# Performance work log

Hardware: AMD Instinct MI355X
Metric: run time of the kernel (lower is better)

## Reference

```python
import jax, jax.numpy as jnp
import numpy as np

B, T, D, H, DH, M, L, OUT = 512, 49, 256, 8, 32, 1024, 4, 151
DI = H * DH
THR = 0.02


def _ln(x, g, b):
    mu = x.mean(-1, keepdims=True)
    v = ((x - mu) ** 2).mean(-1, keepdims=True)
    return (x - mu) / jnp.sqrt(v + 1e-5) * g + b


def setup_inputs() -> dict:
    key = jax.random.key(0)
    ks = iter(jax.random.split(key, 64))

    def W(*s):
        return jax.random.normal(next(ks), s, jnp.float32) * 0.02

    inp = {}
    for n in ['img0', 'img1', 'p0', 'p1', 'p2']:
        inp[n] = jax.random.normal(next(ks), (B, T, D), jnp.float32)
    inp['idx'] = jax.random.randint(next(ks), (3, 2, B, T), 0, T, dtype=jnp.int32)
    # two transformer encoders (image/point), stacked over [encoder=2, layer=L]
    inp['enc_ln1g'] = jnp.ones((2, L, D)); inp['enc_ln1b'] = jnp.zeros((2, L, D))
    inp['enc_wqkv'] = W(2, L, D, 3 * DI)
    inp['enc_wo'] = W(2, L, DI, D); inp['enc_bo'] = jnp.zeros((2, L, D))
    inp['enc_ln2g'] = jnp.ones((2, L, D)); inp['enc_ln2b'] = jnp.zeros((2, L, D))
    inp['enc_w1'] = W(2, L, D, M); inp['enc_b1'] = jnp.zeros((2, L, M))
    inp['enc_w2'] = W(2, L, M, D); inp['enc_b2'] = jnp.zeros((2, L, D))
    # per-depth score nets (PredictorLG)
    inp['sc_lng'] = jnp.ones((L, D)); inp['sc_lnb'] = jnp.zeros((L, D))
    inp['sc_w1'] = W(L, D, D); inp['sc_b1'] = jnp.zeros((L, D))
    inp['sc_w2'] = W(L, D, D // 2); inp['sc_b2'] = jnp.zeros((L, D // 2))
    inp['sc_w3'] = W(L, D // 2, 2); inp['sc_b3'] = jnp.zeros((L, 2))
    # per-depth patch MLPs (FFN dim->mlp_dim->mlp_dim->dim, 3 layers)
    inp['pm_w1'] = W(L, D, M); inp['pm_b1'] = jnp.zeros((L, M))
    inp['pm_w2'] = W(L, M, M); inp['pm_b2'] = jnp.zeros((L, M))
    inp['pm_w3'] = W(L, M, D); inp['pm_b3'] = jnp.zeros((L, D))
    # mlp head
    inp['hd_lng'] = jnp.ones((D,)); inp['hd_lnb'] = jnp.zeros((D,))
    inp['hd_w1'] = W(D, M); inp['hd_b1'] = jnp.zeros((M,))
    inp['hd_w2'] = W(M, OUT); inp['hd_b2'] = jnp.zeros((OUT,))
    return inp


def reference(img0, img1, p0, p1, p2, idx,
              enc_ln1g, enc_ln1b, enc_wqkv, enc_wo, enc_bo,
              enc_ln2g, enc_ln2b, enc_w1, enc_b1, enc_w2, enc_b2,
              sc_lng, sc_lnb, sc_w1, sc_b1, sc_w2, sc_b2, sc_w3, sc_b3,
              pm_w1, pm_b1, pm_w2, pm_b2, pm_w3, pm_b3,
              hd_lng, hd_lnb, hd_w1, hd_b1, hd_w2, hd_b2):

    def layer(x, e, i):
        # pre-norm attention
        h = _ln(x, enc_ln1g[e, i], enc_ln1b[e, i])
        qkv = h @ enc_wqkv[e, i]                      # [B,T,3*DI]
        q, k, v = jnp.split(qkv, 3, axis=-1)
        q = q.reshape(B, T, H, DH); k = k.reshape(B, T, H, DH); v = v.reshape(B, T, H, DH)
        a = jax.nn.softmax(jnp.einsum('bqhd,bkhd->bhqk', q, k) * (DH ** -0.5), -1)
        o = jnp.einsum('bhqk,bkhd->bqhd', a, v).reshape(B, T, DI)
        x = x + o @ enc_wo[e, i] + enc_bo[e, i]
        # pre-norm FFN
        h = _ln(x, enc_ln2g[e, i], enc_ln2b[e, i])
        return x + jax.nn.gelu(h @ enc_w1[e, i] + enc_b1[e, i]) @ enc_w2[e, i] + enc_b2[e, i]

    image_feats = [img0, img1]
    point_feats = [p0, p1, p2]
    pred_scores = []
    for i in range(L):
        image_tokens = [layer(f, 0, i) for f in image_feats]
        point_tokens = [layer(f, 1, i) for f in point_feats]
        allt = jnp.concatenate(image_tokens + point_tokens, axis=1)  # [B, 5*T, D]
        h = _ln(allt, sc_lng[i], sc_lnb[i])
        h = jax.nn.gelu(h @ sc_w1[i] + sc_b1[i])
        h = jax.nn.gelu(h @ sc_w2[i] + sc_b2[i])
        scores = jax.nn.softmax(h @ sc_w3[i] + sc_b3[i], -1)[:, :, 0]  # [B, 5*T]
        pred_scores.append(scores)
        mask = (scores > THR).astype(jnp.int32)[..., None]            # [B,5*T,1]
        fm = mask.astype(allt.dtype)
        fnm = (-mask - 1).astype(allt.dtype)  # torch ~int_mask is bitwise NOT: ~1=-2, ~0=-1 (faithful)
        image_feats = [image_tokens[j] * fm[:, j * T:(j + 1) * T]
                       + image_tokens[1 - j] * fnm[:, j * T:(j + 1) * T] for j in range(2)]

        def patch_mlp(x):
            h2 = jax.nn.gelu(x @ pm_w1[i] + pm_b1[i])
            h2 = jax.nn.gelu(h2 @ pm_w2[i] + pm_b2[i])
            return h2 @ pm_w3[i] + pm_b3[i]

        new_p = []
        for k2 in range(3):
            s0 = 2 * T + k2 * T
            g0 = jnp.take_along_axis(image_tokens[0], idx[k2, 0][..., None], axis=1)
            g1 = jnp.take_along_axis(image_tokens[1], idx[k2, 1][..., None], axis=1)
            patch = patch_mlp(g0) + patch_mlp(g1)
            new_p.append(point_tokens[k2] * fm[:, s0:s0 + T] + patch * fnm[:, s0:s0 + T])
        point_feats = new_p

    pooled = jnp.concatenate(image_feats + point_feats, axis=1).max(axis=1)  # [B, D]
    h = _ln(pooled, hd_lng, hd_lnb)
    smplx = jax.nn.gelu(h @ hd_w1 + hd_b1) @ hd_w2 + hd_b2                   # [B, OUT]
    pred_score = jnp.concatenate(pred_scores, axis=1)                         # [B, L*5*T]
    return smplx, pred_score
```

## Files before the change

### kernel.cpp

```cpp
#include <hip/hip_runtime.h>
#include <math.h>

#define B_ 512
#define T_ 49
#define D_ 256
#define M_ 1024
#define L_ 4
#define OUT_ 151
#define BT_ 25088
#define NTOK5 (5*BT_)
#define THRESH 0.02f

typedef __bf16 bf16x8 __attribute__((ext_vector_type(8)));
typedef float f32x4 __attribute__((ext_vector_type(4)));
typedef unsigned short us;

__device__ __forceinline__ float gelu_t(float x){
    float u = 0.7978845608028654f * x * (1.0f + 0.044715f*x*x);
    float e = __expf(-2.0f*u);
    return __fdividef(x, 1.0f + e);
}
__device__ __forceinline__ us f2bf(float f){
    unsigned int u = __float_as_uint(f);
    u += 0x7fffu + ((u>>16)&1u);
    return (us)(u>>16);
}
__device__ __forceinline__ float bf2f(us h){
    return __uint_as_float(((unsigned int)h)<<16);
}
__device__ __forceinline__ void gload16(const void* g, void* l){
    __builtin_amdgcn_global_load_lds(
        (const __attribute__((address_space(1))) void*)g,
        (__attribute__((address_space(3))) void*)l, 16, 0, 0);
}

__global__ void copy_in_kernel(const float* __restrict__ a0, const float* __restrict__ a1,
                               const float* __restrict__ a2, const float* __restrict__ a3,
                               const float* __restrict__ a4, float* __restrict__ dst){
    size_t i = (size_t)blockIdx.x*256 + threadIdx.x;
    if (i >= (size_t)NTOK5*64) return;
    int slot = (int)(i / ((size_t)BT_*64));
    size_t off = i % ((size_t)BT_*64);
    const float* src = slot==0?a0: slot==1?a1: slot==2?a2: slot==3?a3: a4;
    ((float4*)dst)[i] = ((const float4*)src)[off];
}

__global__ void xcvt_kernel(const float* __restrict__ x, us* __restrict__ y, int nrows){
    size_t i = (size_t)blockIdx.x*256 + threadIdx.x;
    if (i >= (size_t)nrows*64) return;
    float4 v = ((const float4*)x)[i];
    ushort4 o; o.x=f2bf(v.x); o.y=f2bf(v.y); o.z=f2bf(v.z); o.w=f2bf(v.w);
    ((ushort4*)y)[i] = o;
}

template<bool OBF>
__global__ void ln_kernel(const float* __restrict__ x, const float* __restrict__ g,
                          const float* __restrict__ b, void* __restrict__ y, int nrows){
    int row = blockIdx.x*4 + (threadIdx.x>>6);
    if (row >= nrows) return;
    int lane = threadIdx.x & 63;
    float4 v = ((const float4*)(x + (size_t)row*D_))[lane];
    float s  = v.x+v.y+v.z+v.w;
    float sq = v.x*v.x + v.y*v.y + v.z*v.z + v.w*v.w;
    #pragma unroll
    for (int o=32;o;o>>=1){ s += __shfl_xor(s,o,64); sq += __shfl_xor(sq,o,64); }
    float mu = s*(1.0f/256.0f);
    float rstd = rsqrtf(sq*(1.0f/256.0f) - mu*mu + 1e-5f);
    float4 gv = ((const float4*)g)[lane];
    float4 bv = ((const float4*)b)[lane];
    float o0 = (v.x-mu)*rstd*gv.x + bv.x;
    float o1 = (v.y-mu)*rstd*gv.y + bv.y;
    float o2 = (v.z-mu)*rstd*gv.z + bv.z;
    float o3 = (v.w-mu)*rstd*gv.w + bv.w;
    if (OBF){
        ushort4 o4; o4.x=f2bf(o0); o4.y=f2bf(o1); o4.z=f2bf(o2); o4.w=f2bf(o3);
        ((ushort4*)((us*)y + (size_t)row*D_))[lane] = o4;
    } else {
        float4 o4; o4.x=o0; o4.y=o1; o4.z=o2; o4.w=o3;
        ((float4*)((float*)y + (size_t)row*D_))[lane] = o4;
    }
}

__global__ void wtrans_kernel(const float* __restrict__ W, us* __restrict__ Wt,
                              int K, int N){
    int g = blockIdx.z;
    __shared__ float t[32][33];
    int k0 = blockIdx.y*32, n0 = blockIdx.x*32;
    int tx = threadIdx.x&31, ty = threadIdx.x>>5;
    for (int r=ty; r<32; r+=8){
        int k = k0+r, n = n0+tx;
        t[r][tx] = (k<K && n<N) ? W[(size_t)g*K*N + (size_t)k*N + n] : 0.f;
    }
    __syncthreads();
    for (int r=ty; r<32; r+=8){
        int n = n0+r, k = k0+tx;
        if (n<N && k<K) Wt[(size_t)g*N*K + (size_t)n*K + k] = f2bf(t[tx][r]);
    }
}

__global__ void wtrans_pad_kernel(const float* __restrict__ W, us* __restrict__ Wt,
                                  int K, int Nsrc, int Ndst){
    __shared__ float t[32][33];
    int k0 = blockIdx.y*32, n0 = blockIdx.x*32;
    int tx = threadIdx.x&31, ty = threadIdx.x>>5;
    for (int r=ty; r<32; r+=8){
        int k = k0+r, n = n0+tx;
        t[r][tx] = (k<K && n<Nsrc) ? W[(size_t)k*Nsrc + n] : 0.f;
    }
    __syncthreads();
    for (int r=ty; r<32; r+=8){
        int n = n0+r, k = k0+tx;
        if (n<Ndst && k<K) Wt[(size_t)n*K + k] = f2bf(t[tx][r]);
    }
}

__global__ void padb_kernel(const float* __restrict__ b, float* __restrict__ o,
                            int Nsrc, int Ndst){
    int i = blockIdx.x*256 + threadIdx.x;
    if (i < Ndst) o[i] = (i < Nsrc) ? b[i] : 0.f;
}

__global__ void headcopy_kernel(const float* __restrict__ src, float* __restrict__ dst){
    int i = blockIdx.x*256 + threadIdx.x;
    if (i >= B_*OUT_) return;
    int r = i / OUT_, c = i % OUT_;
    dst[i] = src[(size_t)r*256 + c];
}

__device__ __forceinline__ void gemm_compute(const us* As, const us* Bs,
        int wr, int wc, int lr, int kg, f32x4 (&acc)[4][4]){
    bf16x8 av[4], bv[4];
    #pragma unroll
    for (int mi=0;mi<4;mi++){
        int r = wr*64 + mi*16 + lr;
        av[mi] = *(const bf16x8*)(&As[r*32 + ((kg ^ ((r>>1)&3))<<3)]);
    }
    #pragma unroll
    for (int ni=0;ni<4;ni++){
        int c = wc*64 + ni*16 + lr;
        bv[ni] = *(const bf16x8*)(&Bs[c*32 + ((kg ^ ((c>>1)&3))<<3)]);
    }
    #pragma unroll
    for (int mi=0;mi<4;mi++)
        #pragma unroll
        for (int ni=0;ni<4;ni++)
            acc[mi][ni] = __builtin_amdgcn_mfma_f32_16x16x32_bf16(av[mi], bv[ni], acc[mi][ni], 0, 0, 0);
}

template<int ACT, int RIN, bool OBF>
__global__ __launch_bounds__(256) void mfma_gemm(
    const us* __restrict__ A, const us* __restrict__ Wt,
    const float* __restrict__ bias, const void* __restrict__ resid,
    void* __restrict__ Cout, int Mr, int N, int K)
{
    __shared__ __align__(16) us SM[2*8192];
    const int nwg  = gridDim.x*gridDim.y;
    const int flat = blockIdx.y*gridDim.x + blockIdx.x;
    const int qq = nwg>>3, rr = nwg&7;
    const int xcd = flat&7, sidx = flat>>3;
    const int logical = (xcd<rr) ? (xcd*(qq+1)+sidx) : (rr*(qq+1)+(xcd-rr)*qq+sidx);
    const int bn = (logical % gridDim.x)*128;
    const int bm = (logical / gridDim.x)*128;
    const int tid = threadIdx.x;
    const int lane = tid&63, w = tid>>6;
    const int wr = w>>1, wc = w&1;
    const int lr = lane&15, kg = lane>>4;
    f32x4 acc[4][4] = {};

    const int j0 = tid, j1 = tid+256;
    const int row0 = j0>>2, row1 = j1>>2;
    const int k8s0 = (j0&3) ^ ((row0>>1)&3);
    const int k8s1 = (j1&3) ^ ((row1>>1)&3);
    int ga0 = bm+row0; if (ga0>=Mr) ga0=Mr-1;
    int ga1 = bm+row1; if (ga1>=Mr) ga1=Mr-1;
    int gb0 = bn+row0; if (gb0>=N) gb0=N-1;
    int gb1 = bn+row1; if (gb1>=N) gb1=N-1;
    const us* a0p = A  + (size_t)ga0*K + k8s0*8;
    const us* a1p = A  + (size_t)ga1*K + k8s1*8;
    const us* b0p = Wt + (size_t)gb0*K + k8s0*8;
    const us* b1p = Wt + (size_t)gb1*K + k8s1*8;

    const int nk = K >> 5;
    {
        us* b0 = SM;
        gload16(a0p, b0 + j0*8);
        gload16(a1p, b0 + j1*8);
        gload16(b0p, b0 + 4096 + j0*8);
        gload16(b1p, b0 + 4096 + j1*8);
        us* b1 = SM + 8192;
        gload16(a0p+32, b1 + j0*8);
        gload16(a1p+32, b1 + j1*8);
        gload16(b0p+32, b1 + 4096 + j0*8);
        gload16(b1p+32, b1 + 4096 + j1*8);
    }
    int cur = 0;
    for (int t=0; t<nk-1; ++t){
        asm volatile("s_waitcnt vmcnt(4)" ::: "memory");
        __builtin_amdgcn_s_barrier();
        __builtin_amdgcn_sched_barrier(0);
        const us* cbase = SM + cur*8192;
        gemm_compute(cbase, cbase+4096, wr, wc, lr, kg, acc);
        __builtin_amdgcn_sched_barrier(0);
        __builtin_amdgcn_s_barrier();
        if (t+2 < nk){
            us* nbase = SM + cur*8192;
            int k0 = (t+2)<<5;
            gload16(a0p+k0, nbase + j0*8);
            gload16(a1p+k0, nbase + j1*8);
            gload16(b0p+k0, nbase + 4096 + j0*8);
            gload16(b1p+k0, nbase + 4096 + j1*8);
        }
        cur ^= 1;
    }
    asm volatile("s_waitcnt vmcnt(0)" ::: "memory");
    __builtin_amdgcn_s_barrier();
    __builtin_amdgcn_sched_barrier(0);
    {
        const us* cbase = SM + cur*8192;
        gemm_compute(cbase, cbase+4096, wr, wc, lr, kg, acc);
    }
    __syncthreads();

    if (OBF && RIN==0){
        us* Cs16 = (us*)SM;
        #pragma unroll
        for (int mi=0;mi<4;mi++){
            #pragma unroll
            for (int ni=0;ni<4;ni++){
                #pragma unroll
                for (int r4=0;r4<4;r4++){
                    int row = wr*64 + mi*16 + kg*4 + r4;
                    int col = wc*64 + ni*16 + lr;
                    float v = acc[mi][ni][r4];
                    if (bias) v += bias[bn + col];
                    if (ACT==1) v = gelu_t(v);
                    int h = ((row>>2)&3) | ((row&1)<<2);
                    int punit = (col>>3) ^ h;
                    Cs16[row*128 + punit*8 + (col&7)] = f2bf(v);
                }
            }
        }
        __syncthreads();
        {
            int rbase = tid>>3, seg = tid&7;
            #pragma unroll
            for (int pass=0; pass<8; ++pass){
                int row = rbase + (pass>>1)*32;
                int half = pass&1;
                int grow = bm + row;
                if (grow < Mr){
                    int h = ((row>>2)&3) | ((row&1)<<2);
                    int punit = (half*8+seg) ^ h;
                    *(uint4*)((us*)Cout + (size_t)grow*N + bn + half*64 + seg*8)
                        = *(const uint4*)&Cs16[row*128 + punit*8];
                }
            }
        }
        return;
    }

    float* Cs = (float*)SM;
    #pragma unroll
    for (int er=0; er<2; er++){
        #pragma unroll
        for (int ml=0; ml<2; ml++){
            int mi = er*2 + ml;
            #pragma unroll
            for (int ni=0;ni<4;ni++){
                #pragma unroll
                for (int r4=0;r4<4;r4++){
                    int lrow = wr*32 + ml*16 + kg*4 + r4;
                    int lcol = wc*64 + ni*16 + lr;
                    int pcol = lcol ^ (((lrow>>2)&1)<<4);
                    float v = acc[mi][ni][r4];
                    if (bias) v += bias[bn + lcol];
                    if (ACT==1) v = gelu_t(v);
                    Cs[lrow*128 + pcol] = v;
                }
            }
        }
        __syncthreads();
        #pragma unroll
        for (int s=0; s<2; s++){
            int lrow = (tid>>3) + s*32;
            int tseg = tid&7;
            int pseg = tseg ^ ((lrow>>2)&1);
            const float4* src = (const float4*)&Cs[lrow*128 + pseg*16];
            float4 v0=src[0], v1=src[1], v2=src[2], v3=src[3];
            int grow = bm + (lrow>>5)*64 + (er*2 + ((lrow>>4)&1))*16 + (lrow&15);
            int gcol = bn + tseg*16;
            if (grow < Mr){
                if (RIN==1){
                    const float4* rp = (const float4*)((const float*)resid + (size_t)grow*N + gcol);
                    float4 r0=rp[0], r1=rp[1], r2=rp[2], r3=rp[3];
                    v0.x+=r0.x; v0.y+=r0.y; v0.z+=r0.z; v0.w+=r0.w;
                    v1.x+=r1.x; v1.y+=r1.y; v1.z+=r1.z; v1.w+=r1.w;
                    v2.x+=r2.x; v2.y+=r2.y; v2.z+=r2.z; v2.w+=r2.w;
                    v3.x+=r3.x; v3.y+=r3.y; v3.z+=r3.z; v3.w+=r3.w;
                } else if (RIN==2){
                    const uint4* rp = (const uint4*)((const us*)resid + (size_t)grow*N + gcol);
                    uint4 u0=rp[0], u1=rp[1];
                    v0.x+=bf2f((us)(u0.x&0xffff)); v0.y+=bf2f((us)(u0.x>>16));
                    v0.z+=bf2f((us)(u0.y&0xffff)); v0.w+=bf2f((us)(u0.y>>16));
                    v1.x+=bf2f((us)(u0.z&0xffff)); v1.y+=bf2f((us)(u0.z>>16));
                    v1.z+=bf2f((us)(u0.w&0xffff)); v1.w+=bf2f((us)(u0.w>>16));
                    v2.x+=bf2f((us)(u1.x&0xffff)); v2.y+=bf2f((us)(u1.x>>16));
                    v2.z+=bf2f((us)(u1.y&0xffff)); v2.w+=bf2f((us)(u1.y>>16));
                    v3.x+=bf2f((us)(u1.z&0xffff)); v3.y+=bf2f((us)(u1.z>>16));
                    v3.z+=bf2f((us)(u1.w&0xffff)); v3.w+=bf2f((us)(u1.w>>16));
                }
                if (OBF){
                    unsigned int w0 = (unsigned)f2bf(v0.x) | ((unsigned)f2bf(v0.y)<<16);
                    unsigned int w1 = (unsigned)f2bf(v0.z) | ((unsigned)f2bf(v0.w)<<16);
                    unsigned int w2 = (unsigned)f2bf(v1.x) | ((unsigned)f2bf(v1.y)<<16);
                    unsigned int w3 = (unsigned)f2bf(v1.z) | ((unsigned)f2bf(v1.w)<<16);
                    unsigned int w4 = (unsigned)f2bf(v2.x) | ((unsigned)f2bf(v2.y)<<16);
                    unsigned int w5 = (unsigned)f2bf(v2.z) | ((unsigned)f2bf(v2.w)<<16);
                    unsigned int w6 = (unsigned)f2bf(v3.x) | ((unsigned)f2bf(v3.y)<<16);
                    unsigned int w7 = (unsigned)f2bf(v3.z) | ((unsigned)f2bf(v3.w)<<16);
                    uint4* op = (uint4*)((us*)Cout + (size_t)grow*N + gcol);
                    uint4 u0; u0.x=w0; u0.y=w1; u0.z=w2; u0.w=w3;
                    uint4 u1; u1.x=w4; u1.y=w5; u1.z=w6; u1.w=w7;
                    op[0]=u0; op[1]=u1;
                } else {
                    float4* op = (float4*)((float*)Cout + (size_t)grow*N + gcol);
                    op[0]=v0; op[1]=v1; op[2]=v2; op[3]=v3;
                }
            }
        }
        __syncthreads();
    }
}

__global__ void attn_kernel(const us* __restrict__ qkv, us* __restrict__ o){
    int bb = blockIdx.x >> 3;
    int h  = blockIdx.x & 7;
    __shared__ float qs[49][33], ks[49][33], vs[49][33];
    __shared__ float ss[49][49];
    const us* base = qkv + (size_t)bb*T_*768 + h*32;
    for (int i = threadIdx.x; i < 49*16; i += 256){
        int t = i>>4, d2 = i&15;
        unsigned int q = *(const unsigned int*)(base + (size_t)t*768 + d2*2);
        unsigned int k = *(const unsigned int*)(base + (size_t)t*768 + 256 + d2*2);
        unsigned int v = *(const unsigned int*)(base + (size_t)t*768 + 512 + d2*2);
        qs[t][d2*2] = bf2f((us)(q&0xffff)); qs[t][d2*2+1] = bf2f((us)(q>>16));
        ks[t][d2*2] = bf2f((us)(k&0xffff)); ks[t][d2*2+1] = bf2f((us)(k>>16));
        vs[t][d2*2] = bf2f((us)(v&0xffff)); vs[t][d2*2+1] = bf2f((us)(v>>16));
    }
    __syncthreads();
    for (int i = threadIdx.x; i < 49*49; i += 256){
        int r = i/49, c = i%49;
        float acc = 0.f;
        #pragma unroll
        for (int d=0;d<32;d++) acc += qs[r][d]*ks[c][d];
        ss[r][c] = acc*0.17677669529663687f;
    }
    __syncthreads();
    if (threadIdx.x < 196){
        int r = threadIdx.x>>2, q = threadIdx.x&3;
        float m = -1e30f;
        for (int c=q; c<49; c+=4) m = fmaxf(m, ss[r][c]);
        m = fmaxf(m, __shfl_xor(m,1,64)); m = fmaxf(m, __shfl_xor(m,2,64));
        float sum = 0.f;
        for (int c=q; c<49; c+=4){ float e = __expf(ss[r][c]-m); ss[r][c]=e; sum+=e; }
        sum += __shfl_xor(sum,1,64); sum += __shfl_xor(sum,2,64);
        float inv = __fdividef(1.0f, sum);
        for (int c=q; c<49; c+=4) ss[r][c] *= inv;
    }
    __syncthreads();
    for (int i = threadIdx.x; i < 49*32; i += 256){
        int r = i>>5, d = i&31;
        float acc = 0.f;
        for (int c=0;c<49;c++) acc += ss[r][c]*vs[c][d];
        o[((size_t)bb*T_ + r)*256 + h*32 + d] = f2bf(acc);
    }
}

__global__ void score_kernel(const us* __restrict__ s2, const float* __restrict__ w3,
                             const float* __restrict__ b3, float* __restrict__ sc,
                             float* __restrict__ pred, int layer, int row0, int nrows){
    int lr = blockIdx.x*256 + threadIdx.x;
    if (lr >= nrows) return;
    int row = row0 + lr;
    int s = row / BT_;
    int r = row % BT_;
    int b = r / T_;
    int t = r % T_;
    const uint4* xv = (const uint4*)(s2 + (size_t)lr*128);
    float l0 = b3[0], l1 = b3[1];
    #pragma unroll
    for (int q=0;q<16;q++){
        uint4 u = xv[q];
        unsigned int uu[4] = {u.x,u.y,u.z,u.w};
        #pragma unroll
        for (int e=0;e<4;e++){
            float fa = bf2f((us)(uu[e]&0xffff));
            float fb = bf2f((us)(uu[e]>>16));
            int d = q*8 + e*2;
            l0 += fa*w3[d*2]     + fb*w3[(d+1)*2];
            l1 += fa*w3[d*2+1]   + fb*w3[(d+1)*2+1];
        }
    }
    float m = fmaxf(l0,l1);
    float e0 = __expf(l0-m), e1 = __expf(l1-m);
    float sc0 = __fdividef(e0, e0+e1);
    sc[b*(5*T_) + s*T_ + t] = sc0;
    pred[(size_t)b*(L_*5*T_) + (size_t)layer*(5*T_) + s*T_ + t] = sc0;
}

__global__ void img_fuse_kernel(float* __restrict__ X, const float* __restrict__ sc){
    size_t i = (size_t)blockIdx.x*256 + threadIdx.x;
    if (i >= (size_t)BT_*64) return;
    int row = (int)(i>>6), d4 = (int)(i&63);
    int b = row / T_, t = row % T_;
    float s0 = sc[b*(5*T_) + t];
    float s1 = sc[b*(5*T_) + T_ + t];
    float fm0  = (s0 > THRESH)? 1.f : 0.f;
    float fnm0 = -fm0 - 1.f;
    float fm1  = (s1 > THRESH)? 1.f : 0.f;
    float fnm1 = -fm1 - 1.f;
    float4* p0 = ((float4*)(X + (size_t)row*D_)) + d4;
    float4* p1 = ((float4*)(X + ((size_t)BT_ + row)*D_)) + d4;
    float4 a0 = *p0, a1 = *p1;
    float4 r0, r1;
    r0.x = a0.x*fm0 + a1.x*fnm0;  r0.y = a0.y*fm0 + a1.y*fnm0;
    r0.z = a0.z*fm0 + a1.z*fnm0;  r0.w = a0.w*fm0 + a1.w*fnm0;
    r1.x = a1.x*fm1 + a0.x*fnm1;  r1.y = a1.y*fm1 + a0.y*fnm1;
    r1.z = a1.z*fm1 + a0.z*fnm1;  r1.w = a1.w*fm1 + a0.w*fnm1;
    *p0 = r0; *p1 = r1;
}

__global__ void pt_fuse_gather_kernel(float* __restrict__ X, const us* __restrict__ PM,
                                      const int* __restrict__ idx, const float* __restrict__ sc){
    size_t i = (size_t)blockIdx.x*256 + threadIdx.x;
    if (i >= (size_t)3*BT_*64) return;
    int vrow = (int)(i>>6), d4 = (int)(i&63);
    int k2 = vrow / BT_, grow = vrow % BT_;
    int b = grow / T_, t = grow % T_;
    float s = sc[b*(5*T_) + (2+k2)*T_ + t];
    float fm  = (s > THRESH)? 1.f : 0.f;
    float fnm = -fm - 1.f;
    int i0 = idx[(size_t)(k2*2+0)*BT_ + grow];
    int i1 = idx[(size_t)(k2*2+1)*BT_ + grow];
    uint2 u0 = ((const uint2*)(PM + ((size_t)b*T_ + i0)*D_))[d4];
    uint2 u1 = ((const uint2*)(PM + ((size_t)BT_ + (size_t)b*T_ + i1)*D_))[d4];
    float p0 = bf2f((us)(u0.x&0xffff)) + bf2f((us)(u1.x&0xffff));
    float p1 = bf2f((us)(u0.x>>16))    + bf2f((us)(u1.x>>16));
    float p2 = bf2f((us)(u0.y&0xffff)) + bf2f((us)(u1.y&0xffff));
    float p3 = bf2f((us)(u0.y>>16))    + bf2f((us)(u1.y>>16));
    float4* xp = ((float4*)(X + ((size_t)(2+k2)*BT_ + grow)*D_)) + d4;
    float4 a = *xp;
    float4 rr;
    rr.x = a.x*fm + p0*fnm;
    rr.y = a.y*fm + p1*fnm;
    rr.z = a.z*fm + p2*fnm;
    rr.w = a.w*fm + p3*fnm;
    *xp = rr;
}

__global__ void pool_kernel(const float* __restrict__ x, float* __restrict__ p){
    int i = blockIdx.x*256 + threadIdx.x;
    if (i >= B_*64) return;
    int b = i>>6, d4 = i&63;
    float4 m; m.x=m.y=m.z=m.w=-3.4e38f;
    for (int s=0;s<5;s++){
        const float4* bp = ((const float4*)(x + ((size_t)s*BT_ + (size_t)b*T_)*D_)) + d4;
        for (int t=0;t<T_;t++){
            float4 v = bp[(size_t)t*64];
            m.x=fmaxf(m.x,v.x); m.y=fmaxf(m.y,v.y); m.z=fmaxf(m.z,v.z); m.w=fmaxf(m.w,v.w);
        }
    }
    ((float4*)p)[i] = m;
}

static inline int cdiv(int a, int b){ return (a+b-1)/b; }

extern "C" void kernel_launch(void* const* d_in, const int* in_sizes, int n_in,
                              void* d_out, int out_size, void* d_ws, size_t ws_size,
                              hipStream_t stream)
{
    const float* in_img0 = (const float*)d_in[0];
    const float* in_img1 = (const float*)d_in[1];
    const float* in_p0   = (const float*)d_in[2];
    const float* in_p1   = (const float*)d_in[3];
    const float* in_p2   = (const float*)d_in[4];
    const int*   in_idx  = (const int*)d_in[5];
    const float* enc_ln1g = (const float*)d_in[6];
    const float* enc_ln1b = (const float*)d_in[7];
    const float* enc_wqkv = (const float*)d_in[8];
    const float* enc_wo   = (const float*)d_in[9];
    const float* enc_bo   = (const float*)d_in[10];
    const float* enc_ln2g = (const float*)d_in[11];
    const float* enc_ln2b = (const float*)d_in[12];
    const float* enc_w1   = (const float*)d_in[13];
    const float* enc_b1   = (const float*)d_in[14];
    const float* enc_w2   = (const float*)d_in[15];
    const float* enc_b2   = (const float*)d_in[16];
    const float* sc_lng   = (const float*)d_in[17];
    const float* sc_lnb   = (const float*)d_in[18];
    const float* sc_w1    = (const float*)d_in[19];
    const float* sc_b1    = (const float*)d_in[20];
    const float* sc_w2    = (const float*)d_in[21];
    const float* sc_b2    = (const float*)d_in[22];
    const float* sc_w3    = (const float*)d_in[23];
    const float* sc_b3    = (const float*)d_in[24];
    const float* pm_w1    = (const float*)d_in[25];
    const float* pm_b1    = (const float*)d_in[26];
    const float* pm_w2    = (const float*)d_in[27];
    const float* pm_b2    = (const float*)d_in[28];
    const float* pm_w3    = (const float*)d_in[29];
    const float* pm_b3    = (const float*)d_in[30];
    const float* hd_lng   = (const float*)d_in[31];
    const float* hd_lnb   = (const float*)d_in[32];
    const float* hd_w1    = (const float*)d_in[33];
    const float* hd_b1    = (const float*)d_in[34];
    const float* hd_w2    = (const float*)d_in[35];
    const float* hd_b2    = (const float*)d_in[36];

    char* p = (char*)d_ws;
    float* X   = (float*)p;  p += (size_t)5*BT_*D_*4;
    float* SCb = (float*)p;  p += (size_t)B_*5*T_*4;
    us* PM   = (us*)p; p += (size_t)2*BT_*D_*2;
    us* WQKV = (us*)p; p += (size_t)8*768*256*2;
    us* WWO  = (us*)p; p += (size_t)8*256*256*2;
    us* WW1  = (us*)p; p += (size_t)8*1024*256*2;
    us* WW2  = (us*)p; p += (size_t)8*256*1024*2;
    us* WS1  = (us*)p; p += (size_t)4*256*256*2;
    us* WS2  = (us*)p; p += (size_t)4*128*256*2;
    us* WP1  = (us*)p; p += (size_t)4*1024*256*2;
    us* WP2  = (us*)p; p += (size_t)4*1024*1024*2;
    us* WP3  = (us*)p; p += (size_t)4*256*1024*2;
    us* WH1  = (us*)p; p += (size_t)1024*256*2;
    us* WH2  = (us*)p; p += (size_t)256*1024*2;
    float* B2P  = (float*)p; p += (size_t)256*4;
    float* POOL = (float*)p; p += (size_t)B_*256*4;
    us*    HLNb = (us*)p;  p += (size_t)B_*256*2;
    us*    HMIDb= (us*)p;  p += (size_t)B_*1024*2;
    float* HOUT = (float*)p; p += (size_t)B_*256*4;
    size_t fixed = (size_t)(p - (char*)d_ws);
    long long pool = (long long)ws_size - (long long)fixed;
    if (pool < 0) pool = 0;
    auto chunkOf = [&](long long perRow, int maxRows)->int{
        long long c = pool / perRow;
        c = (c / T_) * T_;
        if (c < T_) c = T_;
        if (c > maxRows) c = maxRows;
        return (int)c;
    };
    int Cenc = chunkOf(3072, 3*BT_);
    int Csc  = chunkOf(1280, NTOK5);
    int Cpm  = chunkOf(4608, 2*BT_);
    char* pb = p;
    us* eR1 = (us*)pb;
    us* eR2 = (us*)(pb + (size_t)Cenc*512);
    us* eR3 = (us*)(pb + (size_t)Cenc*512 + (size_t)Cenc*2048);
    us* sR1 = (us*)pb;
    us* sS1 = (us*)(pb + (size_t)Csc*512);
    us* sS2 = (us*)(pb + (size_t)Csc*1024);
    us* cA  = (us*)pb;
    us* m1  = (us*)(pb + (size_t)Cpm*512);
    us* m2  = (us*)(pb + (size_t)Cpm*512 + (size_t)Cpm*2048);

    float* out_smplx = (float*)d_out;
    float* out_pred  = out_smplx + (size_t)B_*OUT_;

    wtrans_kernel<<<dim3(cdiv(768,32), cdiv(256,32), 8),256,0,stream>>>(enc_wqkv, WQKV, 256, 768);
    wtrans_kernel<<<dim3(cdiv(256,32), cdiv(256,32), 8),256,0,stream>>>(enc_wo,   WWO,  256, 256);
    wtrans_kernel<<<dim3(cdiv(1024,32),cdiv(256,32), 8),256,0,stream>>>(enc_w1,   WW1,  256, 1024);
    wtrans_kernel<<<dim3(cdiv(256,32), cdiv(1024,32),8),256,0,stream>>>(enc_w2,   WW2,  1024,256);
    wtrans_kernel<<<dim3(cdiv(256,32), cdiv(256,32), 4),256,0,stream>>>(sc_w1,    WS1,  256, 256);
    wtrans_kernel<<<dim3(cdiv(128,32), cdiv(256,32), 4),256,0,stream>>>(sc_w2,    WS2,  256, 128);
    wtrans_kernel<<<dim3(cdiv(1024,32),cdiv(256,32), 4),256,0,stream>>>(pm_w1,    WP1,  256, 1024);
    wtrans_kernel<<<dim3(cdiv(1024,32),cdiv(1024,32),4),256,0,stream>>>(pm_w2,    WP2,  1024,1024);
    wtrans_kernel<<<dim3(cdiv(256,32), cdiv(1024,32),4),256,0,stream>>>(pm_w3,    WP3,  1024,256);
    wtrans_kernel<<<dim3(cdiv(1024,32),cdiv(256,32), 1),256,0,stream>>>(hd_w1,    WH1,  256, 1024);
    wtrans_pad_kernel<<<dim3(cdiv(256,32), cdiv(1024,32)),256,0,stream>>>(hd_w2, WH2, 1024, 151, 256);
    padb_kernel<<<1,256,0,stream>>>(hd_b2, B2P, 151, 256);

    copy_in_kernel<<<cdiv(NTOK5*64,256), 256, 0, stream>>>(in_img0,in_img1,in_p0,in_p1,in_p2, X);

    for (int i=0;i<L_;i++){
        for (int grp=0; grp<2; grp++){
            int base  = (grp==0)? 0 : 2*BT_;
            int total = (grp==0)? 2*BT_ : 3*BT_;
            size_t wi = (size_t)(grp*L_ + i);
            for (int off=0; off<total; off+=Cenc){
                int R = total-off < Cenc ? total-off : Cenc;
                float* Xp = X + (size_t)(base+off)*D_;
                ln_kernel<true><<<cdiv(R,4),256,0,stream>>>(Xp, enc_ln1g+wi*D_, enc_ln1b+wi*D_, eR1, R);
                mfma_gemm<0,0,true><<<dim3(6, cdiv(R,128)),256,0,stream>>>(
                    eR1, WQKV + wi*768*256, nullptr, nullptr, eR2, R, 768, 256);
                attn_kernel<<<(R/T_)*8,256,0,stream>>>(eR2, eR3);
                mfma_gemm<0,1,false><<<dim3(2, cdiv(R,128)),256,0,stream>>>(
                    eR3, WWO + wi*256*256, enc_bo + wi*D_, Xp, Xp, R, 256, 256);
                ln_kernel<true><<<cdiv(R,4),256,0,stream>>>(Xp, enc_ln2g+wi*D_, enc_ln2b+wi*D_, eR1, R);
                mfma_gemm<1,0,true><<<dim3(8, cdiv(R,128)),256,0,stream>>>(
                    eR1, WW1 + wi*1024*256, enc_b1 + wi*M_, nullptr, eR2, R, 1024, 256);
                mfma_gemm<0,1,false><<<dim3(2, cdiv(R,128)),256,0,stream>>>(
                    eR2, WW2 + wi*256*1024, enc_b2 + wi*D_, Xp, Xp, R, 256, 1024);
            }
        }
        for (int off=0; off<NTOK5; off+=Csc){
            int R = NTOK5-off < Csc ? NTOK5-off : Csc;
            ln_kernel<true><<<cdiv(R,4),256,0,stream>>>(X + (size_t)off*D_,
                sc_lng+(size_t)i*D_, sc_lnb+(size_t)i*D_, sR1, R);
            mfma_gemm<1,0,true><<<dim3(2, cdiv(R,128)),256,0,stream>>>(
                sR1, WS1 + (size_t)i*256*256, sc_b1+(size_t)i*D_, nullptr, sS1, R, 256, 256);
            mfma_gemm<1,0,true><<<dim3(1, cdiv(R,128)),256,0,stream>>>(
                sS1, WS2 + (size_t)i*128*256, sc_b2+(size_t)i*128, nullptr, sS2, R, 128, 256);
            score_kernel<<<cdiv(R,256),256,0,stream>>>(
                sS2, sc_w3+(size_t)i*256, sc_b3+(size_t)i*2, SCb, out_pred, i, off, R);
        }
        for (int off=0; off<2*BT_; off+=Cpm){
            int R = 2*BT_-off < Cpm ? 2*BT_-off : Cpm;
            xcvt_kernel<<<cdiv(R*64,256),256,0,stream>>>(X + (size_t)off*D_, cA, R);
            mfma_gemm<1,0,true><<<dim3(8, cdiv(R,128)),256,0,stream>>>(
                cA, WP1 + (size_t)i*1024*256, pm_b1+(size_t)i*M_, nullptr, m1, R, 1024, 256);
            mfma_gemm<1,0,true><<<dim3(8, cdiv(R,128)),256,0,stream>>>(
                m1, WP2 + (size_t)i*1024*1024, pm_b2+(size_t)i*M_, nullptr, m2, R, 1024, 1024);
            mfma_gemm<0,0,true><<<dim3(2, cdiv(R,128)),256,0,stream>>>(
                m2, WP3 + (size_t)i*256*1024, pm_b3+(size_t)i*D_, nullptr, PM + (size_t)off*D_, R, 256, 1024);
        }
        pt_fuse_gather_kernel<<<cdiv(3*BT_*64,256),256,0,stream>>>(X, PM, in_idx, SCb);
        img_fuse_kernel<<<cdiv(BT_*64,256),256,0,stream>>>(X, SCb);
    }
    pool_kernel<<<cdiv(B_*64,256),256,0,stream>>>(X, POOL);
    ln_kernel<true><<<cdiv(B_,4),256,0,stream>>>(POOL, hd_lng, hd_lnb, HLNb, B_);
    mfma_gemm<1,0,true><<<dim3(8, cdiv(B_,128)),256,0,stream>>>(
        HLNb, WH1, hd_b1, nullptr, HMIDb, B_, 1024, 256);
    mfma_gemm<0,0,false><<<dim3(2, cdiv(B_,128)),256,0,stream>>>(
        HMIDb, WH2, B2P, nullptr, HOUT, B_, 256, 1024);
    headcopy_kernel<<<cdiv(B_*OUT_,256),256,0,stream>>>(HOUT, out_smplx);
}
```

Measured before the change: 6.693 ms.

## Rewrite attention as one-row-per-lane kernel and alias scratch buffers for larger chunks

Attention now runs one wavefront per (batch, head), with each lane owning one query row in registers. Only K and V are staged in shared memory, which removes the score matrix in shared memory and two block barriers. Scratch buffers are aliased (attention output reuses the LN buffer, score output reuses its input, and the patch-MLP input shares with m2), so less memory is needed per row and larger chunks fit in the workspace. Chunk sizes are also balanced so the last chunk is not tiny. The cost is heavy register use (S[49], q[32], oa[32]) and 15 idle lanes per wavefront.

```diff
diff --git a/kernel.cpp b/kernel.cpp
--- a/kernel.cpp
+++ b/kernel.cpp
@@ -332,48 +332,73 @@
     }
 }
 
-__global__ void attn_kernel(const us* __restrict__ qkv, us* __restrict__ o){
-    int bb = blockIdx.x >> 3;
-    int h  = blockIdx.x & 7;
-    __shared__ float qs[49][33], ks[49][33], vs[49][33];
-    __shared__ float ss[49][49];
+__global__ __launch_bounds__(128) void attn_kernel(const us* __restrict__ qkv,
+                                                   us* __restrict__ o){
+    __shared__ float ks[2][T_][36], vs[2][T_][36];
+    const int w = threadIdx.x >> 6, lane = threadIdx.x & 63;
+    const int bh = blockIdx.x*2 + w;
+    const int bb = bh >> 3, h = bh & 7;
     const us* base = qkv + (size_t)bb*T_*768 + h*32;
-    for (int i = threadIdx.x; i < 49*16; i += 256){
-        int t = i>>4, d2 = i&15;
-        unsigned int q = *(const unsigned int*)(base + (size_t)t*768 + d2*2);
-        unsigned int k = *(const unsigned int*)(base + (size_t)t*768 + 256 + d2*2);
-        unsigned int v = *(const unsigned int*)(base + (size_t)t*768 + 512 + d2*2);
-        qs[t][d2*2] = bf2f((us)(q&0xffff)); qs[t][d2*2+1] = bf2f((us)(q>>16));
-        ks[t][d2*2] = bf2f((us)(k&0xffff)); ks[t][d2*2+1] = bf2f((us)(k>>16));
-        vs[t][d2*2] = bf2f((us)(v&0xffff)); vs[t][d2*2+1] = bf2f((us)(v>>16));
+    if (lane < T_){
+        const uint4* kp = (const uint4*)(base + (size_t)lane*768 + 256);
+        const uint4* vp = (const uint4*)(base + (size_t)lane*768 + 512);
+        #pragma unroll
+        for (int j=0;j<4;j++){
+            uint4 ku = kp[j], vu = vp[j];
+            unsigned ka[4]={ku.x,ku.y,ku.z,ku.w}, va[4]={vu.x,vu.y,vu.z,vu.w};
+            #pragma unroll
+            for (int e=0;e<4;e++){
+                ks[w][lane][j*8+e*2]   = bf2f((us)(ka[e]&0xffffu));
+                ks[w][lane][j*8+e*2+1] = bf2f((us)(ka[e]>>16));
+                vs[w][lane][j*8+e*2]   = bf2f((us)(va[e]&0xffffu));
+                vs[w][lane][j*8+e*2+1] = bf2f((us)(va[e]>>16));
+            }
+        }
     }
     __syncthreads();
-    for (int i = threadIdx.x; i < 49*49; i += 256){
-        int r = i/49, c = i%49;
+    if (lane >= T_) return;
+    float q[32];
+    {
+        const uint4* qp = (const uint4*)(base + (size_t)lane*768);
+        #pragma unroll
+        for (int j=0;j<4;j++){
+            uint4 qu = qp[j];
+            unsigned qa[4]={qu.x,qu.y,qu.z,qu.w};
+            #pragma unroll
+            for (int e=0;e<4;e++){
+                q[j*8+e*2]   = bf2f((us)(qa[e]&0xffffu));
+                q[j*8+e*2+1] = bf2f((us)(qa[e]>>16));
+            }
+        }
+    }
+    float S[T_];
+    #pragma unroll
+    for (int c=0;c<T_;c++){
         float acc = 0.f;
         #pragma unroll
-        for (int d=0;d<32;d++) acc += qs[r][d]*ks[c][d];
-        ss[r][c] = acc*0.17677669529663687f;
-    }
-    __syncthreads();
-    if (threadIdx.x < 196){
-        int r = threadIdx.x>>2, q = threadIdx.x&3;
-        float m = -1e30f;
-        for (int c=q; c<49; c+=4) m = fmaxf(m, ss[r][c]);
-        m = fmaxf(m, __shfl_xor(m,1,64)); m = fmaxf(m, __shfl_xor(m,2,64));
-        float sum = 0.f;
-        for (int c=q; c<49; c+=4){ float e = __expf(ss[r][c]-m); ss[r][c]=e; sum+=e; }
-        sum += __shfl_xor(sum,1,64); sum += __shfl_xor(sum,2,64);
-        float inv = __fdividef(1.0f, sum);
-        for (int c=q; c<49; c+=4) ss[r][c] *= inv;
-    }
-    __syncthreads();
-    for (int i = threadIdx.x; i < 49*32; i += 256){
-        int r = i>>5, d = i&31;
-        float acc = 0.f;
-        for (int c=0;c<49;c++) acc += ss[r][c]*vs[c][d];
-        o[((size_t)bb*T_ + r)*256 + h*32 + d] = f2bf(acc);
-    }
+        for (int d=0;d<32;d++) acc += q[d]*ks[w][c][d];
+        S[c] = acc*0.17677669529663687f;
+    }
+    float m = S[0];
+    #pragma unroll
+    for (int c=1;c<T_;c++) m = fmaxf(m, S[c]);
+    float sum = 0.f;
+    #pragma unroll
+    for (int c=0;c<T_;c++){ S[c] = __expf(S[c]-m); sum += S[c]; }
+    float inv = __fdividef(1.f, sum);
+    float oa[32];
+    #pragma unroll
+    for (int d=0;d<32;d++) oa[d] = 0.f;
+    #pragma unroll
+    for (int c=0;c<T_;c++){
+        float p2 = S[c]*inv;
+        #pragma unroll
+        for (int d=0;d<32;d++) oa[d] += p2*vs[w][c][d];
+    }
+    unsigned* op = (unsigned*)(o + ((size_t)bb*T_ + lane)*256 + h*32);
+    #pragma unroll
+    for (int j=0;j<16;j++)
+        op[j] = (unsigned)f2bf(oa[2*j]) | ((unsigned)f2bf(oa[2*j+1])<<16);
 }
 
 __global__ void score_kernel(const us* __restrict__ s2, const float* __restrict__ w3,
@@ -538,28 +563,35 @@
     us*    HMIDb= (us*)p;  p += (size_t)B_*1024*2;
     float* HOUT = (float*)p; p += (size_t)B_*256*4;
     size_t fixed = (size_t)(p - (char*)d_ws);
-    long long pool = (long long)ws_size - (long long)fixed;
-    if (pool < 0) pool = 0;
+    long long poolb = (long long)ws_size - (long long)fixed;
+    if (poolb < 0) poolb = 0;
     auto chunkOf = [&](long long perRow, int maxRows)->int{
-        long long c = pool / perRow;
+        long long c = poolb / perRow;
         c = (c / T_) * T_;
         if (c < T_) c = T_;
         if (c > maxRows) c = maxRows;
         return (int)c;
     };
-    int Cenc = chunkOf(3072, 3*BT_);
-    int Csc  = chunkOf(1280, NTOK5);
-    int Cpm  = chunkOf(4608, 2*BT_);
+    auto evenC = [&](int total, int Cmax)->int{
+        int nch = (total + Cmax - 1)/Cmax;
+        int per = (total + nch - 1)/nch;
+        per = ((per + T_ - 1)/T_)*T_;
+        if (per > Cmax) per = Cmax;
+        return per;
+    };
+    int CencMax = chunkOf(2560, 3*BT_);
+    int CscMax  = chunkOf(1024, NTOK5);
+    int CpmMax  = chunkOf(4096, 2*BT_);
     char* pb = p;
     us* eR1 = (us*)pb;
-    us* eR2 = (us*)(pb + (size_t)Cenc*512);
-    us* eR3 = (us*)(pb + (size_t)Cenc*512 + (size_t)Cenc*2048);
+    us* eR2 = (us*)(pb + (size_t)CencMax*512);
+    us* eR3 = eR1;
     us* sR1 = (us*)pb;
-    us* sS1 = (us*)(pb + (size_t)Csc*512);
-    us* sS2 = (us*)(pb + (size_t)Csc*1024);
-    us* cA  = (us*)pb;
-    us* m1  = (us*)(pb + (size_t)Cpm*512);
-    us* m2  = (us*)(pb + (size_t)Cpm*512 + (size_t)Cpm*2048);
+    us* sS1 = (us*)(pb + (size_t)CscMax*512);
+    us* sS2 = sR1;
+    us* m1  = (us*)pb;
+    us* m2  = (us*)(pb + (size_t)CpmMax*2048);
+    us* cA  = m2;
 
     float* out_smplx = (float*)d_out;
     float* out_pred  = out_smplx + (size_t)B_*OUT_;
@@ -584,13 +616,14 @@
             int base  = (grp==0)? 0 : 2*BT_;
             int total = (grp==0)? 2*BT_ : 3*BT_;
             size_t wi = (size_t)(grp*L_ + i);
-            for (int off=0; off<total; off+=Cenc){
-                int R = total-off < Cenc ? total-off : Cenc;
+            int C = evenC(total, CencMax);
+            for (int off=0; off<total; off+=C){
+                int R = total-off < C ? total-off : C;
                 float* Xp = X + (size_t)(base+off)*D_;
                 ln_kernel<true><<<cdiv(R,4),256,0,stream>>>(Xp, enc_ln1g+wi*D_, enc_ln1b+wi*D_, eR1, R);
                 mfma_gemm<0,0,true><<<dim3(6, cdiv(R,128)),256,0,stream>>>(
                     eR1, WQKV + wi*768*256, nullptr, nullptr, eR2, R, 768, 256);
-                attn_kernel<<<(R/T_)*8,256,0,stream>>>(eR2, eR3);
+                attn_kernel<<<(R/T_)*4,128,0,stream>>>(eR2, eR3);
                 mfma_gemm<0,1,false><<<dim3(2, cdiv(R,128)),256,0,stream>>>(
                     eR3, WWO + wi*256*256, enc_bo + wi*D_, Xp, Xp, R, 256, 256);
                 ln_kernel<true><<<cdiv(R,4),256,0,stream>>>(Xp, enc_ln2g+wi*D_, enc_ln2b+wi*D_, eR1, R);
@@ -600,26 +633,32 @@
                     eR2, WW2 + wi*256*1024, enc_b2 + wi*D_, Xp, Xp, R, 256, 1024);
             }
         }
-        for (int off=0; off<NTOK5; off+=Csc){
-            int R = NTOK5-off < Csc ? NTOK5-off : Csc;
-            ln_kernel<true><<<cdiv(R,4),256,0,stream>>>(X + (size_t)off*D_,
-                sc_lng+(size_t)i*D_, sc_lnb+(size_t)i*D_, sR1, R);
-            mfma_gemm<1,0,true><<<dim3(2, cdiv(R,128)),256,0,stream>>>(
-                sR1, WS1 + (size_t)i*256*256, sc_b1+(size_t)i*D_, nullptr, sS1, R, 256, 256);
-            mfma_gemm<1,0,true><<<dim3(1, cdiv(R,128)),256,0,stream>>>(
-                sS1, WS2 + (size_t)i*128*256, sc_b2+(size_t)i*128, nullptr, sS2, R, 128, 256);
-            score_kernel<<<cdiv(R,256),256,0,stream>>>(
-                sS2, sc_w3+(size_t)i*256, sc_b3+(size_t)i*2, SCb, out_pred, i, off, R);
-        }
-        for (int off=0; off<2*BT_; off+=Cpm){
-            int R = 2*BT_-off < Cpm ? 2*BT_-off : Cpm;
-            xcvt_kernel<<<cdiv(R*64,256),256,0,stream>>>(X + (size_t)off*D_, cA, R);
-            mfma_gemm<1,0,true><<<dim3(8, cdiv(R,128)),256,0,stream>>>(
-                cA, WP1 + (size_t)i*1024*256, pm_b1+(size_t)i*M_, nullptr, m1, R, 1024, 256);
-            mfma_gemm<1,0,true><<<dim3(8, cdiv(R,128)),256,0,stream>>>(
-                m1, WP2 + (size_t)i*1024*1024, pm_b2+(size_t)i*M_, nullptr, m2, R, 1024, 1024);
-            mfma_gemm<0,0,true><<<dim3(2, cdiv(R,128)),256,0,stream>>>(
-                m2, WP3 + (size_t)i*256*1024, pm_b3+(size_t)i*D_, nullptr, PM + (size_t)off*D_, R, 256, 1024);
+        {
+            int C = evenC(NTOK5, CscMax);
+            for (int off=0; off<NTOK5; off+=C){
+                int R = NTOK5-off < C ? NTOK5-off : C;
+                ln_kernel<true><<<cdiv(R,4),256,0,stream>>>(X + (size_t)off*D_,
+                    sc_lng+(size_t)i*D_, sc_lnb+(size_t)i*D_, sR1, R);
+                mfma_gemm<1,0,true><<<dim3(2, cdiv(R,128)),256,0,stream>>>(
+                    sR1, WS1 + (size_t)i*256*256, sc_b1+(size_t)i*D_, nullptr, sS1, R, 256, 256);
+                mfma_gemm<1,0,true><<<dim3(1, cdiv(R,128)),256,0,stream>>>(
+                    sS1, WS2 + (size_t)i*128*256, sc_b2+(size_t)i*128, nullptr, sS2, R, 128, 256);
+                score_kernel<<<cdiv(R,256),256,0,stream>>>(
+                    sS2, sc_w3+(size_t)i*256, sc_b3+(size_t)i*2, SCb, out_pred, i, off, R);
+            }
+        }
+        {
+            int C = evenC(2*BT_, CpmMax);
+            for (int off=0; off<2*BT_; off+=C){
+                int R = 2*BT_-off < C ? 2*BT_-off : C;
+                xcvt_kernel<<<cdiv(R*64,256),256,0,stream>>>(X + (size_t)off*D_, cA, R);
+                mfma_gemm<1,0,true><<<dim3(8, cdiv(R,128)),256,0,stream>>>(
+                    cA, WP1 + (size_t)i*1024*256, pm_b1+(size_t)i*M_, nullptr, m1, R, 1024, 256);
+                mfma_gemm<1,0,true><<<dim3(8, cdiv(R,128)),256,0,stream>>>(
+                    m1, WP2 + (size_t)i*1024*1024, pm_b2+(size_t)i*M_, nullptr, m2, R, 1024, 1024);
+                mfma_gemm<0,0,true><<<dim3(2, cdiv(R,128)),256,0,stream>>>(
+                    m2, WP3 + (size_t)i*256*1024, pm_b3+(size_t)i*D_, nullptr, PM + (size_t)off*D_, R, 256, 1024);
+            }
         }
         pt_fuse_gather_kernel<<<cdiv(3*BT_*64,256),256,0,stream>>>(X, PM, in_idx, SCb);
         img_fuse_kernel<<<cdiv(BT_*64,256),256,0,stream>>>(X, SCb);
```

Measured after the change: 6.089 ms (median of 2 runs). 9.0% less time.
